# Optimization experiments

Hardware: AMD Instinct MI355X
Metric: run time of the kernel (lower is better)

Reference implementation:

```python
import jax, jax.numpy as jnp
import numpy as np

NEG_SLOPE = 0.01  # torch LeakyReLU default

def leaky_relu(x):
    return jnp.where(x >= 0, x, NEG_SLOPE * x)

def gcn_conv(h, W, b, src, dst, n):
    # PyG GCNConv: linear (no bias), add self-loops, symmetric norm, scatter-add, + bias
    h = h @ W  # [N, F]
    loop = jnp.arange(n, dtype=src.dtype)
    s = jnp.concatenate([src, loop])
    d = jnp.concatenate([dst, loop])
    deg = jax.ops.segment_sum(jnp.ones_like(d, dtype=h.dtype), d, num_segments=n)
    dinv = jnp.where(deg > 0, deg ** -0.5, 0.0)
    norm = dinv[s] * dinv[d]  # [E+N]
    msg = h[s] * norm[:, None]
    out = jax.ops.segment_sum(msg, d, num_segments=n)
    return out + b

def setup_inputs() -> dict:
    key = jax.random.key(0)
    ks = jax.random.split(key, 12)
    N, E, D_IN, D_H, D_OUT, C = 100000, 3200000, 512, 128, 64, 2
    def lin(k, fi, fo):
        bound = 1.0 / np.sqrt(fi)
        k1, k2 = jax.random.split(k)
        W = jax.random.uniform(k1, (fi, fo), jnp.float32, -bound, bound)
        b = jax.random.uniform(k2, (fo,), jnp.float32, -bound, bound)
        return W, b
    W1, b1 = lin(ks[0], D_IN, D_H)
    W2, b2 = lin(ks[1], D_H, D_OUT)
    Wg1, bg1 = lin(ks[2], D_OUT, D_OUT)
    Wg2, bg2 = lin(ks[3], D_OUT, D_OUT)
    Wc, bc = lin(ks[4], D_OUT, C)
    x = jax.random.normal(ks[5], (N, D_IN), jnp.float32)
    edge_index = jax.random.randint(ks[6], (2, E), 0, N, jnp.int32)
    return {"x": x, "edge_index": edge_index, "W1": W1, "b1": b1, "W2": W2, "b2": b2,
            "Wg1": Wg1, "bg1": bg1, "Wg2": Wg2, "bg2": bg2, "Wc": Wc, "bc": bc}

def reference(x, edge_index, W1, b1, W2, b2, Wg1, bg1, Wg2, bg2, Wc, bc):
    n = x.shape[0]
    src, dst = edge_index[0], edge_index[1]
    # encoder (dropout = identity in eval)
    h = leaky_relu(x @ W1 + b1)
    h = leaky_relu(h @ W2 + b2)
    # two GCN layers
    h = leaky_relu(gcn_conv(h, Wg1, bg1, src, dst, n))
    h = leaky_relu(gcn_conv(h, Wg2, bg2, src, dst, n))
    logits = h @ Wc + bc
    return logits, h
```

## Files before the change

kernel.cpp:

```cpp
#include <hip/hip_runtime.h>
#include <hip/hip_bf16.h>

typedef __bf16 v8bf16 __attribute__((ext_vector_type(8)));
typedef float  v4f32  __attribute__((ext_vector_type(4)));
typedef unsigned short ushort8v __attribute__((ext_vector_type(8)));

static __device__ __forceinline__ float leaky(float v) { return v >= 0.0f ? v : 0.01f * v; }
static __device__ __forceinline__ float bfbits2f(unsigned short b) {
    union { unsigned u; float f; } c; c.u = ((unsigned)b) << 16; return c.f;
}
static __device__ __forceinline__ unsigned short f2bfbits(float f) {
    __hip_bfloat16 h = __float2bfloat16(f);
    unsigned short s; __builtin_memcpy(&s, &h, 2); return s;
}

__global__ void prep_frag(const float* __restrict__ W, __hip_bfloat16* __restrict__ out,
                          int K, int N, int total) {
    int tid = blockIdx.x * 256 + threadIdx.x;
    if (tid >= total) return;
    int j = tid & 7, l = (tid >> 3) & 63, G = tid >> 9;
    int m = l & 15, q = l >> 4;
    int t = G & 7, kk = G >> 3;
    int n = t * 16 + m;
    int k = kk * 32 + q * 8 + j;
    out[tid] = __float2bfloat16(W[k * N + n]);
}

__global__ void prep_small(const float* __restrict__ W2, const float* __restrict__ Wg1,
                           const float* __restrict__ Wg2, __hip_bfloat16* __restrict__ W2t,
                           __hip_bfloat16* __restrict__ Wg1t, __hip_bfloat16* __restrict__ Wg2t,
                           int DH, int DO) {
    const int n2 = DH * DO, ng = DO * DO;
    int i = blockIdx.x * 256 + threadIdx.x;
    if (i < n2) {
        int r = i / DO, c = i % DO;
        W2t[c * DH + r] = __float2bfloat16(W2[i]);
    } else if (i < n2 + ng) {
        int j = i - n2; int r = j / DO, c = j % DO;
        Wg1t[c * DO + r] = __float2bfloat16(Wg1[j]);
    } else if (i < n2 + 2 * ng) {
        int j = i - n2 - ng; int r = j / DO, c = j % DO;
        Wg2t[c * DO + r] = __float2bfloat16(Wg2[j]);
    }
}

__global__ void zero_u32(unsigned* __restrict__ p, int n) {
    int i = blockIdx.x * 256 + threadIdx.x;
    if (i < n) p[i] = 0u;
}

constexpr int EPB  = 6400;
constexpr int BCAP = 16384;

__global__ __launch_bounds__(512) void bucket_scatter(
    const int* __restrict__ src, const int* __restrict__ dst,
    unsigned* __restrict__ bcur, unsigned* __restrict__ ebuck, int E, int NB) {
    __shared__ unsigned stg[EPB];
    __shared__ unsigned hist[512], inc[512], cur[512], start[512];
    const int tid = threadIdx.x;
    hist[tid] = 0u;
    __syncthreads();
    const int beg = blockIdx.x * EPB;
    const int end = min(beg + EPB, E);
    for (int e = beg + tid; e < end; e += 512)
        atomicAdd(&hist[((unsigned)dst[e]) >> 8], 1u);
    __syncthreads();
    const unsigned h = hist[tid];
    inc[tid] = h;
    __syncthreads();
    for (int off = 1; off < 512; off <<= 1) {
        unsigned t = (tid >= off) ? inc[tid - off] : 0u;
        __syncthreads();
        inc[tid] += t;
        __syncthreads();
    }
    cur[tid] = inc[tid] - h;
    if (tid < NB && h > 0u)
        start[tid] = (unsigned)tid * BCAP + atomicAdd(&bcur[tid], h);
    __syncthreads();
    for (int e = beg + tid; e < end; e += 512) {
        unsigned b = ((unsigned)dst[e]) >> 8;
        unsigned r = atomicAdd(&cur[b], 1u);
        stg[r] = (unsigned)e;
    }
    __syncthreads();
    const int cnt = end - beg;
    for (int s = tid; s < cnt; s += 512) {
        const unsigned e = stg[s];
        const unsigned d = (unsigned)dst[e];
        const unsigned b = d >> 8;
        const unsigned excl = inc[b] - hist[b];
        const unsigned pos = start[b] + ((unsigned)s - excl);
        ebuck[pos] = (unsigned)src[e] | ((d & 255u) << 20);
    }
}

__global__ __launch_bounds__(512) void bucket_scan(const unsigned* __restrict__ bcnt,
                                                   unsigned* __restrict__ bases, int NB) {
    __shared__ unsigned ts[512];
    const int tid = threadIdx.x;
    unsigned v = (tid < NB) ? bcnt[tid] : 0u;
    ts[tid] = v;
    __syncthreads();
    for (int off = 1; off < 512; off <<= 1) {
        unsigned t = (tid >= off) ? ts[tid - off] : 0u;
        __syncthreads();
        ts[tid] += t;
        __syncthreads();
    }
    if (tid < NB) {
        bases[tid] = ts[tid] - v;
        if (tid == NB - 1) bases[NB] = ts[tid];
    }
}

__global__ __launch_bounds__(256) void bucket_csr(
    const unsigned* __restrict__ bases, const unsigned* __restrict__ bcnt,
    const unsigned* __restrict__ ebuck, unsigned* __restrict__ rowptr,
    float* __restrict__ dinv, int* __restrict__ csr, int NN) {
    __shared__ unsigned hist[256], cur[256];
    const int tid = threadIdx.x;
    const int k = blockIdx.x;
    const unsigned cntb = bcnt[k];
    const unsigned base = bases[k];
    const unsigned* eb = ebuck + (size_t)k * BCAP;
    hist[tid] = 0u;
    __syncthreads();
    for (unsigned e = tid; e < cntb; e += 256)
        atomicAdd(&hist[eb[e] >> 20], 1u);
    __syncthreads();
    const unsigned h = hist[tid];
    cur[tid] = h;
    __syncthreads();
    for (int off = 1; off < 256; off <<= 1) {
        unsigned t = (tid >= off) ? cur[tid - off] : 0u;
        __syncthreads();
        cur[tid] += t;
        __syncthreads();
    }
    const unsigned excl = cur[tid] - h;
    const int node = k * 256 + tid;
    if (node < NN) {
        rowptr[node] = base + excl;
        if (node == NN - 1) rowptr[NN] = base + excl + h;
        dinv[node] = rsqrtf((float)(h + 1u));
    }
    __syncthreads();
    cur[tid] = excl;
    __syncthreads();
    for (unsigned e = tid; e < cntb; e += 256) {
        const unsigned pk = eb[e];
        const unsigned pos = base + atomicAdd(&cur[pk >> 20], 1u);
        csr[pos] = (int)(pk & 0xFFFFFu);
    }
}

__global__ __launch_bounds__(256, 4) void gemm_enc1(
    const float* __restrict__ A, const uint4* __restrict__ Bp,
    const float* __restrict__ bias, __hip_bfloat16* __restrict__ C, int M) {
    constexpr int K = 512;
    __shared__ uint4 lds[2][1024];
    const int tid = threadIdx.x;
    const int wid = tid >> 6, lane = tid & 63;
    const int m = lane & 15, q = lane >> 4;
    const int row0 = blockIdx.x * 64 + wid * 16;
    const int rowA = row0 + m;
    const int rowAc = rowA < M ? rowA : M - 1;
    const float* Ap = A + (size_t)rowAc * K + q * 8;

    v4f32 acc[8];
#pragma unroll
    for (int t = 0; t < 8; t++) acc[t] = (v4f32){0.f, 0.f, 0.f, 0.f};

    float4 ab[2][4];

    auto loadA = [&](int c, int par) {
#pragma unroll
        for (int j = 0; j < 4; j++)
            ab[par][j] = *reinterpret_cast<const float4*>(Ap + c * 64 + (j >> 1) * 32 + (j & 1) * 4);
    };
    auto stage = [&](int c, int par) {
#pragma unroll
        for (int r = 0; r < 4; r++)
            lds[par][r * 256 + tid] = Bp[c * 1024 + r * 256 + tid];
    };

    stage(0, 0);
    loadA(0, 0);
    for (int c = 0; c < 8; c++) {
        __syncthreads();
        if (c < 7) { stage(c + 1, (c + 1) & 1); loadA(c + 1, (c + 1) & 1); }
        const int par = c & 1;
#pragma unroll
        for (int kk2 = 0; kk2 < 2; kk2++) {
            float4 f0 = ab[par][kk2 * 2], f1 = ab[par][kk2 * 2 + 1];
            v8bf16 a = {(__bf16)f0.x, (__bf16)f0.y, (__bf16)f0.z, (__bf16)f0.w,
                        (__bf16)f1.x, (__bf16)f1.y, (__bf16)f1.z, (__bf16)f1.w};
#pragma unroll
            for (int t = 0; t < 8; t++) {
                v8bf16 b = reinterpret_cast<const v8bf16*>(lds[par])[(kk2 * 8 + t) * 64 + lane];
                acc[t] = __builtin_amdgcn_mfma_f32_16x16x32_bf16(a, b, acc[t], 0, 0, 0);
            }
        }
    }

#pragma unroll
    for (int r = 0; r < 4; r++) {
        const int row = row0 + q * 4 + r;
        if (row >= M) continue;
#pragma unroll
        for (int t = 0; t < 8; t++) {
            const int col = t * 16 + m;
            C[(size_t)row * 128 + col] = __float2bfloat16(leaky(acc[t][r] + bias[col]));
        }
    }
}

template <int NT, int MODE>
__global__ __launch_bounds__(256) void gemm_kernel(
    const __hip_bfloat16* __restrict__ A, const __hip_bfloat16* __restrict__ Bt,
    const float* __restrict__ bias, const float* __restrict__ dinv,
    __hip_bfloat16* __restrict__ Cbf, int M, int K) {
    const int wid  = threadIdx.x >> 6;
    const int lane = threadIdx.x & 63;
    const int row0 = (blockIdx.x * 4 + wid) << 4;
    if (row0 >= M) return;
    const int m = lane & 15, q = lane >> 4;

    const __hip_bfloat16* Ab = A + (size_t)(row0 + m) * K + q * 8;

    v4f32 acc[NT];
#pragma unroll
    for (int t = 0; t < NT; t++) acc[t] = (v4f32){0.f, 0.f, 0.f, 0.f};

    for (int k0 = 0; k0 < K; k0 += 32) {
        v8bf16 a = *reinterpret_cast<const v8bf16*>(Ab + k0);
#pragma unroll
        for (int t = 0; t < NT; t++) {
            v8bf16 b = *reinterpret_cast<const v8bf16*>(Bt + (size_t)(t * 16 + m) * K + k0 + q * 8);
            acc[t] = __builtin_amdgcn_mfma_f32_16x16x32_bf16(a, b, acc[t], 0, 0, 0);
        }
    }

    const int N = NT * 16;
#pragma unroll
    for (int r = 0; r < 4; r++) {
        const int row = row0 + q * 4 + r;
        float di = (MODE == 1) ? dinv[row] : 1.0f;
#pragma unroll
        for (int t = 0; t < NT; t++) {
            const int col = t * 16 + m;
            float v = acc[t][r];
            if (MODE == 0) v = leaky(v + bias[col]);
            else           v *= di;
            Cbf[(size_t)row * N + col] = __float2bfloat16(v);
        }
    }
}

template <int HEAD>
__global__ __launch_bounds__(256) void gather_kernel(
    const unsigned* __restrict__ rowptr, const int* __restrict__ csr_src,
    const __hip_bfloat16* __restrict__ u, const float* __restrict__ dinv,
    const float* __restrict__ bias, __hip_bfloat16* __restrict__ out_bf,
    float* __restrict__ out_h, const float* __restrict__ Wc,
    const float* __restrict__ bc, float* __restrict__ out_logits, int n) {
    const int node = blockIdx.x * 4 + (threadIdx.x >> 6);
    if (node >= n) return;
    const int lane = threadIdx.x & 63;
    const int g = lane >> 3, t = lane & 7;
    const unsigned beg = rowptr[node], end = rowptr[node + 1];

    float s[8];
#pragma unroll
    for (int j = 0; j < 8; j++) s[j] = 0.f;

    unsigned e = beg + g;
    bool have = e < end;
    int sidx = have ? csr_src[e] : 0;
    while (have) {
        const unsigned en = e + 8;
        const bool hn = en < end;
        const int sn = hn ? csr_src[en] : 0;
        ushort8v w = *reinterpret_cast<const ushort8v*>(u + (size_t)sidx * 64 + t * 8);
#pragma unroll
        for (int j = 0; j < 8; j++) s[j] += bfbits2f(w[j]);
        e = en; sidx = sn; have = hn;
    }
#pragma unroll
    for (int j = 0; j < 8; j++) {
        s[j] += __shfl_xor(s[j], 8, 64);
        s[j] += __shfl_xor(s[j], 16, 64);
        s[j] += __shfl_xor(s[j], 32, 64);
    }

    ushort8v wsr = *reinterpret_cast<const ushort8v*>(u + (size_t)node * 64 + t * 8);
#pragma unroll
    for (int j = 0; j < 8; j++) s[j] += bfbits2f(wsr[j]);

    const float di = dinv[node];
    const float4 b0 = *reinterpret_cast<const float4*>(bias + t * 8);
    const float4 b1 = *reinterpret_cast<const float4*>(bias + t * 8 + 4);
    float f[8];
    f[0] = leaky(s[0] * di + b0.x); f[1] = leaky(s[1] * di + b0.y);
    f[2] = leaky(s[2] * di + b0.z); f[3] = leaky(s[3] * di + b0.w);
    f[4] = leaky(s[4] * di + b1.x); f[5] = leaky(s[5] * di + b1.y);
    f[6] = leaky(s[6] * di + b1.z); f[7] = leaky(s[7] * di + b1.w);

    if (HEAD == 0) {
        if (g == 0) {
            ushort8v o;
#pragma unroll
            for (int j = 0; j < 8; j++) o[j] = f2bfbits(f[j]);
            *reinterpret_cast<ushort8v*>(out_bf + (size_t)node * 64 + t * 8) = o;
        }
    } else {
        if (g == 0) {
            float4 o0 = {f[0], f[1], f[2], f[3]};
            float4 o1 = {f[4], f[5], f[6], f[7]};
            *reinterpret_cast<float4*>(out_h + (size_t)node * 64 + t * 8) = o0;
            *reinterpret_cast<float4*>(out_h + (size_t)node * 64 + t * 8 + 4) = o1;
        }
        float p0 = 0.f, p1 = 0.f;
#pragma unroll
        for (int j = 0; j < 8; j++) {
            p0 += f[j] * Wc[(t * 8 + j) * 2];
            p1 += f[j] * Wc[(t * 8 + j) * 2 + 1];
        }
#pragma unroll
        for (int o = 4; o; o >>= 1) {
            p0 += __shfl_xor(p0, o, 64);
            p1 += __shfl_xor(p1, o, 64);
        }
        if (lane == 0) {
            out_logits[(size_t)node * 2 + 0] = p0 + bc[0];
            out_logits[(size_t)node * 2 + 1] = p1 + bc[1];
        }
    }
}

extern "C" void kernel_launch(void* const* d_in, const int* in_sizes, int n_in,
                              void* d_out, int out_size, void* d_ws, size_t ws_size,
                              hipStream_t stream) {
    const float* x   = (const float*)d_in[0];
    const int*   ei  = (const int*)d_in[1];
    const float* W1  = (const float*)d_in[2];
    const float* b1  = (const float*)d_in[3];
    const float* W2  = (const float*)d_in[4];
    const float* b2  = (const float*)d_in[5];
    const float* Wg1 = (const float*)d_in[6];
    const float* bg1 = (const float*)d_in[7];
    const float* Wg2 = (const float*)d_in[8];
    const float* bg2 = (const float*)d_in[9];
    const float* Wc  = (const float*)d_in[10];
    const float* bc  = (const float*)d_in[11];

    const int DH  = in_sizes[3];
    const int DIN = in_sizes[2] / DH;
    const int NN  = in_sizes[0] / DIN;
    const int E   = in_sizes[1] / 2;
    const int DO  = in_sizes[5];
    const int* src = ei;
    const int* dst = ei + E;

    char*  ws  = (char*)d_ws;
    size_t off = 0;
    auto alloc = [&](size_t bytes) {
        void* p = ws + off;
        off += (bytes + 255) & ~(size_t)255;
        return p;
    };
    const int NB = (NN + 255) >> 8;
    __hip_bfloat16* h1    = (__hip_bfloat16*)alloc((size_t)NN * DH * 2);
    __hip_bfloat16* h2    = (__hip_bfloat16*)alloc((size_t)NN * DO * 2);
    __hip_bfloat16* h3    = (__hip_bfloat16*)alloc((size_t)NN * DO * 2);
    __hip_bfloat16* ub    = (__hip_bfloat16*)alloc((size_t)NN * DO * 2);
    float*          dinv  = (float*)alloc((size_t)NN * 4);
    unsigned*       rowp  = (unsigned*)alloc(((size_t)NN + 1) * 4);
    int*            csr   = (int*)alloc((size_t)E * 4);
    unsigned*       ebuck = (unsigned*)alloc((size_t)NB * BCAP * 4);
    unsigned*       bcur  = (unsigned*)alloc(512 * 4);
    unsigned*       bases = (unsigned*)alloc(513 * 4);
    __hip_bfloat16* W1f   = (__hip_bfloat16*)alloc((size_t)DIN * DH * 2);
    __hip_bfloat16* W2t   = (__hip_bfloat16*)alloc((size_t)DH * DO * 2);
    __hip_bfloat16* Wg1t  = (__hip_bfloat16*)alloc((size_t)DO * DO * 2);
    __hip_bfloat16* Wg2t  = (__hip_bfloat16*)alloc((size_t)DO * DO * 2);

    float* out_logits = (float*)d_out;
    float* out_h      = (float*)d_out + (size_t)NN * 2;

    prep_frag<<<(DIN * DH + 255) / 256, 256, 0, stream>>>(W1, W1f, DIN, DH, DIN * DH);
    prep_small<<<(DH * DO + 2 * DO * DO + 255) / 256, 256, 0, stream>>>(
        W2, Wg1, Wg2, W2t, Wg1t, Wg2t, DH, DO);

    const int nblkP = (E + EPB - 1) / EPB;
    zero_u32<<<(NB + 255) / 256, 256, 0, stream>>>(bcur, NB);
    bucket_scatter<<<nblkP, 512, 0, stream>>>(src, dst, bcur, ebuck, E, NB);
    bucket_scan<<<1, 512, 0, stream>>>(bcur, bases, NB);
    bucket_csr<<<NB, 256, 0, stream>>>(bases, bcur, ebuck, rowp, dinv, csr, NN);

    const int gemm_blocks = (NN / 16 + 3) / 4;

    gemm_enc1<<<(NN + 63) / 64, 256, 0, stream>>>(x, (const uint4*)W1f, b1, h1, NN);
    gemm_kernel<4, 0><<<gemm_blocks, 256, 0, stream>>>(h1, W2t, b2, nullptr, h2, NN, DH);

    gemm_kernel<4, 1><<<gemm_blocks, 256, 0, stream>>>(h2, Wg1t, nullptr, dinv, ub, NN, DO);
    gather_kernel<0><<<(NN + 3) / 4, 256, 0, stream>>>(rowp, csr, ub, dinv, bg1, h3,
                                                       nullptr, nullptr, nullptr, nullptr, NN);

    gemm_kernel<4, 1><<<gemm_blocks, 256, 0, stream>>>(h3, Wg2t, nullptr, dinv, ub, NN, DO);
    gather_kernel<1><<<(NN + 3) / 4, 256, 0, stream>>>(rowp, csr, ub, dinv, bg2, nullptr,
                                                       out_h, Wc, bc, out_logits, NN);
}
```

Baseline: 595.5 us.

## Fuse graph-build kernels with encoder GEMMs and drop the bucket scan

```diff
diff --git a/kernel.cpp b/kernel.cpp
--- a/kernel.cpp
+++ b/kernel.cpp
@@ -14,156 +14,102 @@
     unsigned short s; __builtin_memcpy(&s, &h, 2); return s;
 }
 
-__global__ void prep_frag(const float* __restrict__ W, __hip_bfloat16* __restrict__ out,
-                          int K, int N, int total) {
-    int tid = blockIdx.x * 256 + threadIdx.x;
-    if (tid >= total) return;
-    int j = tid & 7, l = (tid >> 3) & 63, G = tid >> 9;
-    int m = l & 15, q = l >> 4;
-    int t = G & 7, kk = G >> 3;
-    int n = t * 16 + m;
-    int k = kk * 32 + q * 8 + j;
-    out[tid] = __float2bfloat16(W[k * N + n]);
-}
-
-__global__ void prep_small(const float* __restrict__ W2, const float* __restrict__ Wg1,
-                           const float* __restrict__ Wg2, __hip_bfloat16* __restrict__ W2t,
-                           __hip_bfloat16* __restrict__ Wg1t, __hip_bfloat16* __restrict__ Wg2t,
-                           int DH, int DO) {
-    const int n2 = DH * DO, ng = DO * DO;
-    int i = blockIdx.x * 256 + threadIdx.x;
-    if (i < n2) {
-        int r = i / DO, c = i % DO;
-        W2t[c * DH + r] = __float2bfloat16(W2[i]);
-    } else if (i < n2 + ng) {
-        int j = i - n2; int r = j / DO, c = j % DO;
-        Wg1t[c * DO + r] = __float2bfloat16(Wg1[j]);
-    } else if (i < n2 + 2 * ng) {
-        int j = i - n2 - ng; int r = j / DO, c = j % DO;
-        Wg2t[c * DO + r] = __float2bfloat16(Wg2[j]);
-    }
-}
-
-__global__ void zero_u32(unsigned* __restrict__ p, int n) {
-    int i = blockIdx.x * 256 + threadIdx.x;
-    if (i < n) p[i] = 0u;
-}
-
 constexpr int EPB  = 6400;
 constexpr int BCAP = 16384;
 
-__global__ __launch_bounds__(512) void bucket_scatter(
-    const int* __restrict__ src, const int* __restrict__ dst,
+__global__ __launch_bounds__(256) void prep_all(
+    const float* __restrict__ W1, const float* __restrict__ W2,
+    const float* __restrict__ Wg1, const float* __restrict__ Wg2,
+    __hip_bfloat16* __restrict__ W1f, __hip_bfloat16* __restrict__ W2t,
+    __hip_bfloat16* __restrict__ Wg1t, __hip_bfloat16* __restrict__ Wg2t,
+    unsigned* __restrict__ bcur, int DIN, int DH, int DO, int NB) {
+    const int fragTotal  = DIN * DH;
+    const int fragBlocks = (fragTotal + 255) / 256;
+    const int n2 = DH * DO, ng = DO * DO;
+    const int smallTotal  = n2 + 2 * ng;
+    const int smallBlocks = (smallTotal + 255) / 256;
+    const int bid = blockIdx.x;
+    if (bid < fragBlocks) {
+        int tid = bid * 256 + threadIdx.x;
+        if (tid >= fragTotal) return;
+        int j = tid & 7, l = (tid >> 3) & 63, G = tid >> 9;
+        int m = l & 15, q = l >> 4;
+        int t = G & 7, kk = G >> 3;
+        int n = t * 16 + m;
+        int k = kk * 32 + q * 8 + j;
+        W1f[tid] = __float2bfloat16(W1[k * DH + n]);
+    } else if (bid < fragBlocks + smallBlocks) {
+        int i = (bid - fragBlocks) * 256 + threadIdx.x;
+        if (i < n2) {
+            int r = i / DO, c = i % DO;
+            W2t[c * DH + r] = __float2bfloat16(W2[i]);
+        } else if (i < n2 + ng) {
+            int j = i - n2; int r = j / DO, c = j % DO;
+            Wg1t[c * DO + r] = __float2bfloat16(Wg1[j]);
+        } else if (i < smallTotal) {
+            int j = i - n2 - ng; int r = j / DO, c = j % DO;
+            Wg2t[c * DO + r] = __float2bfloat16(Wg2[j]);
+        }
+    } else {
+        int i = (bid - fragBlocks - smallBlocks) * 256 + threadIdx.x;
+        if (i < NB) bcur[i] = 0u;
+    }
+}
+
+struct ScatterSmem {
+    unsigned stg[EPB];
+    unsigned hist[512], inc[512], cur[512], start[512];
+};
+
+static __device__ __forceinline__ void scatter_body(
+    int bid, ScatterSmem& sm, const int* __restrict__ src, const int* __restrict__ dst,
     unsigned* __restrict__ bcur, unsigned* __restrict__ ebuck, int E, int NB) {
-    __shared__ unsigned stg[EPB];
-    __shared__ unsigned hist[512], inc[512], cur[512], start[512];
     const int tid = threadIdx.x;
-    hist[tid] = 0u;
-    __syncthreads();
-    const int beg = blockIdx.x * EPB;
+    sm.hist[tid] = 0u;
+    __syncthreads();
+    const int beg = bid * EPB;
     const int end = min(beg + EPB, E);
     for (int e = beg + tid; e < end; e += 512)
-        atomicAdd(&hist[((unsigned)dst[e]) >> 8], 1u);
-    __syncthreads();
-    const unsigned h = hist[tid];
-    inc[tid] = h;
+        atomicAdd(&sm.hist[((unsigned)dst[e]) >> 8], 1u);
+    __syncthreads();
+    const unsigned h = sm.hist[tid];
+    sm.inc[tid] = h;
     __syncthreads();
     for (int off = 1; off < 512; off <<= 1) {
-        unsigned t = (tid >= off) ? inc[tid - off] : 0u;
+        unsigned t = (tid >= off) ? sm.inc[tid - off] : 0u;
         __syncthreads();
-        inc[tid] += t;
+        sm.inc[tid] += t;
         __syncthreads();
     }
-    cur[tid] = inc[tid] - h;
+    sm.cur[tid] = sm.inc[tid] - h;
     if (tid < NB && h > 0u)
-        start[tid] = (unsigned)tid * BCAP + atomicAdd(&bcur[tid], h);
+        sm.start[tid] = (unsigned)tid * BCAP + atomicAdd(&bcur[tid], h);
     __syncthreads();
     for (int e = beg + tid; e < end; e += 512) {
         unsigned b = ((unsigned)dst[e]) >> 8;
-        unsigned r = atomicAdd(&cur[b], 1u);
-        stg[r] = (unsigned)e;
+        unsigned r = atomicAdd(&sm.cur[b], 1u);
+        sm.stg[r] = (unsigned)e;
     }
     __syncthreads();
     const int cnt = end - beg;
     for (int s = tid; s < cnt; s += 512) {
-        const unsigned e = stg[s];
+        const unsigned e = sm.stg[s];
         const unsigned d = (unsigned)dst[e];
         const unsigned b = d >> 8;
-        const unsigned excl = inc[b] - hist[b];
-        const unsigned pos = start[b] + ((unsigned)s - excl);
+        const unsigned excl = sm.inc[b] - sm.hist[b];
+        const unsigned pos = sm.start[b] + ((unsigned)s - excl);
         ebuck[pos] = (unsigned)src[e] | ((d & 255u) << 20);
     }
 }
 
-__global__ __launch_bounds__(512) void bucket_scan(const unsigned* __restrict__ bcnt,
-                                                   unsigned* __restrict__ bases, int NB) {
-    __shared__ unsigned ts[512];
-    const int tid = threadIdx.x;
-    unsigned v = (tid < NB) ? bcnt[tid] : 0u;
-    ts[tid] = v;
-    __syncthreads();
-    for (int off = 1; off < 512; off <<= 1) {
-        unsigned t = (tid >= off) ? ts[tid - off] : 0u;
-        __syncthreads();
-        ts[tid] += t;
-        __syncthreads();
-    }
-    if (tid < NB) {
-        bases[tid] = ts[tid] - v;
-        if (tid == NB - 1) bases[NB] = ts[tid];
-    }
-}
-
-__global__ __launch_bounds__(256) void bucket_csr(
-    const unsigned* __restrict__ bases, const unsigned* __restrict__ bcnt,
-    const unsigned* __restrict__ ebuck, unsigned* __restrict__ rowptr,
-    float* __restrict__ dinv, int* __restrict__ csr, int NN) {
-    __shared__ unsigned hist[256], cur[256];
-    const int tid = threadIdx.x;
-    const int k = blockIdx.x;
-    const unsigned cntb = bcnt[k];
-    const unsigned base = bases[k];
-    const unsigned* eb = ebuck + (size_t)k * BCAP;
-    hist[tid] = 0u;
-    __syncthreads();
-    for (unsigned e = tid; e < cntb; e += 256)
-        atomicAdd(&hist[eb[e] >> 20], 1u);
-    __syncthreads();
-    const unsigned h = hist[tid];
-    cur[tid] = h;
-    __syncthreads();
-    for (int off = 1; off < 256; off <<= 1) {
-        unsigned t = (tid >= off) ? cur[tid - off] : 0u;
-        __syncthreads();
-        cur[tid] += t;
-        __syncthreads();
-    }
-    const unsigned excl = cur[tid] - h;
-    const int node = k * 256 + tid;
-    if (node < NN) {
-        rowptr[node] = base + excl;
-        if (node == NN - 1) rowptr[NN] = base + excl + h;
-        dinv[node] = rsqrtf((float)(h + 1u));
-    }
-    __syncthreads();
-    cur[tid] = excl;
-    __syncthreads();
-    for (unsigned e = tid; e < cntb; e += 256) {
-        const unsigned pk = eb[e];
-        const unsigned pos = base + atomicAdd(&cur[pk >> 20], 1u);
-        csr[pos] = (int)(pk & 0xFFFFFu);
-    }
-}
-
-__global__ __launch_bounds__(256, 4) void gemm_enc1(
-    const float* __restrict__ A, const uint4* __restrict__ Bp,
+static __device__ __forceinline__ void enc1_body(
+    int bid, uint4 (*lds)[1024], const float* __restrict__ A, const uint4* __restrict__ Bp,
     const float* __restrict__ bias, __hip_bfloat16* __restrict__ C, int M) {
     constexpr int K = 512;
-    __shared__ uint4 lds[2][1024];
     const int tid = threadIdx.x;
     const int wid = tid >> 6, lane = tid & 63;
     const int m = lane & 15, q = lane >> 4;
-    const int row0 = blockIdx.x * 64 + wid * 16;
+    const int row0 = bid * 128 + wid * 16;
     const int rowA = row0 + m;
     const int rowAc = rowA < M ? rowA : M - 1;
     const float* Ap = A + (size_t)rowAc * K + q * 8;
@@ -180,9 +126,8 @@
             ab[par][j] = *reinterpret_cast<const float4*>(Ap + c * 64 + (j >> 1) * 32 + (j & 1) * 4);
     };
     auto stage = [&](int c, int par) {
-#pragma unroll
-        for (int r = 0; r < 4; r++)
-            lds[par][r * 256 + tid] = Bp[c * 1024 + r * 256 + tid];
+        lds[par][tid]       = Bp[c * 1024 + tid];
+        lds[par][512 + tid] = Bp[c * 1024 + 512 + tid];
     };
 
     stage(0, 0);
@@ -216,14 +161,29 @@
     }
 }
 
+__global__ __launch_bounds__(512, 4) void mega_scatter_enc1(
+    const int* __restrict__ src, const int* __restrict__ dst,
+    unsigned* __restrict__ bcur, unsigned* __restrict__ ebuck, int E, int NB, int nScatter,
+    const float* __restrict__ A, const uint4* __restrict__ Bp,
+    const float* __restrict__ bias, __hip_bfloat16* __restrict__ C, int M) {
+    union Smem {
+        ScatterSmem sc;
+        uint4 g[2][1024];
+    };
+    __shared__ Smem sm;
+    const int bid = blockIdx.x;
+    if (bid < nScatter) scatter_body(bid, sm.sc, src, dst, bcur, ebuck, E, NB);
+    else                enc1_body(bid - nScatter, sm.g, A, Bp, bias, C, M);
+}
+
 template <int NT, int MODE>
-__global__ __launch_bounds__(256) void gemm_kernel(
-    const __hip_bfloat16* __restrict__ A, const __hip_bfloat16* __restrict__ Bt,
+static __device__ __forceinline__ void gemm_body(
+    int bid, const __hip_bfloat16* __restrict__ A, const __hip_bfloat16* __restrict__ Bt,
     const float* __restrict__ bias, const float* __restrict__ dinv,
     __hip_bfloat16* __restrict__ Cbf, int M, int K) {
     const int wid  = threadIdx.x >> 6;
     const int lane = threadIdx.x & 63;
-    const int row0 = (blockIdx.x * 4 + wid) << 4;
+    const int row0 = (bid * 4 + wid) << 4;
     if (row0 >= M) return;
     const int m = lane & 15, q = lane >> 4;
 
@@ -258,9 +218,67 @@
     }
 }
 
+template <int NT, int MODE>
+__global__ __launch_bounds__(256) void gemm_kernel(
+    const __hip_bfloat16* __restrict__ A, const __hip_bfloat16* __restrict__ Bt,
+    const float* __restrict__ bias, const float* __restrict__ dinv,
+    __hip_bfloat16* __restrict__ Cbf, int M, int K) {
+    gemm_body<NT, MODE>(blockIdx.x, A, Bt, bias, dinv, Cbf, M, K);
+}
+
+static __device__ __forceinline__ void csr_body(
+    int k, unsigned* hist, unsigned* cur, const unsigned* __restrict__ bcur,
+    const unsigned* __restrict__ ebuck, uint2* __restrict__ rp2,
+    float* __restrict__ dinv, int* __restrict__ csr, int NN) {
+    const int tid = threadIdx.x;
+    const unsigned cntb = bcur[k];
+    const unsigned base = (unsigned)k * BCAP;
+    const unsigned* eb = ebuck + base;
+    hist[tid] = 0u;
+    __syncthreads();
+    for (unsigned e = tid; e < cntb; e += 256)
+        atomicAdd(&hist[eb[e] >> 20], 1u);
+    __syncthreads();
+    const unsigned h = hist[tid];
+    cur[tid] = h;
+    __syncthreads();
+    for (int off = 1; off < 256; off <<= 1) {
+        unsigned t = (tid >= off) ? cur[tid - off] : 0u;
+        __syncthreads();
+        cur[tid] += t;
+        __syncthreads();
+    }
+    const unsigned excl = cur[tid] - h;
+    const int node = k * 256 + tid;
+    if (node < NN) {
+        rp2[node] = make_uint2(base + excl, base + excl + h);
+        dinv[node] = rsqrtf((float)(h + 1u));
+    }
+    __syncthreads();
+    cur[tid] = excl;
+    __syncthreads();
+    for (unsigned e = tid; e < cntb; e += 256) {
+        const unsigned pk = eb[e];
+        const unsigned pos = base + atomicAdd(&cur[pk >> 20], 1u);
+        csr[pos] = (int)(pk & 0xFFFFFu);
+    }
+}
+
+__global__ __launch_bounds__(256) void mega_csr_enc2(
+    const unsigned* __restrict__ bcur, const unsigned* __restrict__ ebuck,
+    uint2* __restrict__ rp2, float* __restrict__ dinv, int* __restrict__ csr,
+    int NN, int nCsr,
+    const __hip_bfloat16* __restrict__ A, const __hip_bfloat16* __restrict__ Bt,
+    const float* __restrict__ bias, __hip_bfloat16* __restrict__ Cb, int M, int K) {
+    __shared__ unsigned hist[256], cur[256];
+    const int bid = blockIdx.x;
+    if (bid < nCsr) csr_body(bid, hist, cur, bcur, ebuck, rp2, dinv, csr, NN);
+    else            gemm_body<4, 0>(bid - nCsr, A, Bt, bias, nullptr, Cb, M, K);
+}
+
 template <int HEAD>
 __global__ __launch_bounds__(256) void gather_kernel(
-    const unsigned* __restrict__ rowptr, const int* __restrict__ csr_src,
+    const uint2* __restrict__ rp2, const int* __restrict__ csr_src,
     const __hip_bfloat16* __restrict__ u, const float* __restrict__ dinv,
     const float* __restrict__ bias, __hip_bfloat16* __restrict__ out_bf,
     float* __restrict__ out_h, const float* __restrict__ Wc,
@@ -269,23 +287,32 @@
     if (node >= n) return;
     const int lane = threadIdx.x & 63;
     const int g = lane >> 3, t = lane & 7;
-    const unsigned beg = rowptr[node], end = rowptr[node + 1];
+    const uint2 rp = rp2[node];
+    const unsigned beg = rp.x, end = rp.y;
 
     float s[8];
 #pragma unroll
     for (int j = 0; j < 8; j++) s[j] = 0.f;
 
     unsigned e = beg + g;
-    bool have = e < end;
-    int sidx = have ? csr_src[e] : 0;
-    while (have) {
-        const unsigned en = e + 8;
-        const bool hn = en < end;
-        const int sn = hn ? csr_src[en] : 0;
-        ushort8v w = *reinterpret_cast<const ushort8v*>(u + (size_t)sidx * 64 + t * 8);
-#pragma unroll
-        for (int j = 0; j < 8; j++) s[j] += bfbits2f(w[j]);
-        e = en; sidx = sn; have = hn;
+    bool hA = e < end, hB = e + 8 < end;
+    int sA = hA ? csr_src[e] : 0;
+    int sB = hB ? csr_src[e + 8] : 0;
+    while (hA) {
+        const unsigned en = e + 16;
+        const bool hA2 = en < end, hB2 = en + 8 < end;
+        const int sA2 = hA2 ? csr_src[en] : 0;
+        const int sB2 = hB2 ? csr_src[en + 8] : 0;
+        ushort8v wA = *reinterpret_cast<const ushort8v*>(u + (size_t)sA * 64 + t * 8);
+        if (hB) {
+            ushort8v wB = *reinterpret_cast<const ushort8v*>(u + (size_t)sB * 64 + t * 8);
+#pragma unroll
+            for (int j = 0; j < 8; j++) s[j] += bfbits2f(wA[j]) + bfbits2f(wB[j]);
+        } else {
+#pragma unroll
+            for (int j = 0; j < 8; j++) s[j] += bfbits2f(wA[j]);
+        }
+        e = en; hA = hA2; hB = hB2; sA = sA2; sB = sB2;
     }
 #pragma unroll
     for (int j = 0; j < 8; j++) {
@@ -376,11 +403,10 @@
     __hip_bfloat16* h3    = (__hip_bfloat16*)alloc((size_t)NN * DO * 2);
     __hip_bfloat16* ub    = (__hip_bfloat16*)alloc((size_t)NN * DO * 2);
     float*          dinv  = (float*)alloc((size_t)NN * 4);
-    unsigned*       rowp  = (unsigned*)alloc(((size_t)NN + 1) * 4);
-    int*            csr   = (int*)alloc((size_t)E * 4);
+    uint2*          rp2   = (uint2*)alloc((size_t)NN * 8);
+    int*            csr   = (int*)alloc((size_t)NB * BCAP * 4);
     unsigned*       ebuck = (unsigned*)alloc((size_t)NB * BCAP * 4);
     unsigned*       bcur  = (unsigned*)alloc(512 * 4);
-    unsigned*       bases = (unsigned*)alloc(513 * 4);
     __hip_bfloat16* W1f   = (__hip_bfloat16*)alloc((size_t)DIN * DH * 2);
     __hip_bfloat16* W2t   = (__hip_bfloat16*)alloc((size_t)DH * DO * 2);
     __hip_bfloat16* Wg1t  = (__hip_bfloat16*)alloc((size_t)DO * DO * 2);
@@ -389,26 +415,28 @@
     float* out_logits = (float*)d_out;
     float* out_h      = (float*)d_out + (size_t)NN * 2;
 
-    prep_frag<<<(DIN * DH + 255) / 256, 256, 0, stream>>>(W1, W1f, DIN, DH, DIN * DH);
-    prep_small<<<(DH * DO + 2 * DO * DO + 255) / 256, 256, 0, stream>>>(
-        W2, Wg1, Wg2, W2t, Wg1t, Wg2t, DH, DO);
+    const int fragBlocks  = (DIN * DH + 255) / 256;
+    const int smallBlocks = (DH * DO + 2 * DO * DO + 255) / 256;
+    const int zeroBlocks  = (NB + 255) / 256;
+    prep_all<<<fragBlocks + smallBlocks + zeroBlocks, 256, 0, stream>>>(
+        W1, W2, Wg1, Wg2, W1f, W2t, Wg1t, Wg2t, bcur, DIN, DH, DO, NB);
 
     const int nblkP = (E + EPB - 1) / EPB;
-    zero_u32<<<(NB + 255) / 256, 256, 0, stream>>>(bcur, NB);
-    bucket_scatter<<<nblkP, 512, 0, stream>>>(src, dst, bcur, ebuck, E, NB);
-    bucket_scan<<<1, 512, 0, stream>>>(bcur, bases, NB);
-    bucket_csr<<<NB, 256, 0, stream>>>(bases, bcur, ebuck, rowp, dinv, csr, NN);
+    const int enc1B = (NN + 127) / 128;
+    mega_scatter_enc1<<<nblkP + enc1B, 512, 0, stream>>>(
+        src, dst, bcur, ebuck, E, NB, nblkP,
+        x, (const uint4*)W1f, b1, h1, NN);
 
     const int gemm_blocks = (NN / 16 + 3) / 4;
-
-    gemm_enc1<<<(NN + 63) / 64, 256, 0, stream>>>(x, (const uint4*)W1f, b1, h1, NN);
-    gemm_kernel<4, 0><<<gemm_blocks, 256, 0, stream>>>(h1, W2t, b2, nullptr, h2, NN, DH);
+    mega_csr_enc2<<<NB + gemm_blocks, 256, 0, stream>>>(
+        bcur, ebuck, rp2, dinv, csr, NN, NB,
+        h1, W2t, b2, h2, NN, DH);
 
     gemm_kernel<4, 1><<<gemm_blocks, 256, 0, stream>>>(h2, Wg1t, nullptr, dinv, ub, NN, DO);
-    gather_kernel<0><<<(NN + 3) / 4, 256, 0, stream>>>(rowp, csr, ub, dinv, bg1, h3,
+    gather_kernel<0><<<(NN + 3) / 4, 256, 0, stream>>>(rp2, csr, ub, dinv, bg1, h3,
                                                        nullptr, nullptr, nullptr, nullptr, NN);
 
     gemm_kernel<4, 1><<<gemm_blocks, 256, 0, stream>>>(h3, Wg2t, nullptr, dinv, ub, NN, DO);
-    gather_kernel<1><<<(NN + 3) / 4, 256, 0, stream>>>(rowp, csr, ub, dinv, bg2, nullptr,
+    gather_kernel<1><<<(NN + 3) / 4, 256, 0, stream>>>(rp2, csr, ub, dinv, bg2, nullptr,
                                                        out_h, Wc, bc, out_logits, NN);
 }
```

Result: faster. 557.1 us (-6.4%).
